# Kernel tuning notes

Hardware: AMD Instinct MI355X
Metric: run time of the kernel (lower is better)

The kernel has to match this reference:

```python
import jax, jax.numpy as jnp
import numpy as np

N = 100000  # nodes per cluster
E = 1000000  # nonzeros per sparse Laplacian
D = 64       # embedding_size
LEAKY_SLOPE = 0.2  # tf.nn.leaky_relu default alpha


def spmm(rows, cols, vals, dense, num_rows):
    """Sparse [num_rows, M] (COO) @ dense [M, D] -> [num_rows, D]."""
    gathered = vals[:, None] * dense[cols]  # [E, D]
    return jax.ops.segment_sum(gathered, rows, num_segments=num_rows)


def setup_inputs() -> dict:
    key = jax.random.key(0)
    ks = jax.random.split(key, 10)
    return {
        "ebs": jax.random.normal(ks[0], (N, D), dtype=jnp.float32),
        "entity_ebs": jax.random.normal(ks[1], (N, D), dtype=jnp.float32),
        "W_side": jax.random.normal(ks[2], (D, D), dtype=jnp.float32),
        "W_dot": jax.random.normal(ks[3], (D, D), dtype=jnp.float32),
        "LI_vals": jax.random.uniform(ks[4], (E,), dtype=jnp.float32),
        "L_vals": jax.random.uniform(ks[5], (E,), dtype=jnp.float32),
        "LI_rows": jax.random.randint(ks[6], (E,), 0, N, dtype=jnp.int32),
        "LI_cols": jax.random.randint(ks[7], (E,), 0, N, dtype=jnp.int32),
        "L_rows": jax.random.randint(ks[8], (E,), 0, N, dtype=jnp.int32),
        "L_cols": jax.random.randint(ks[9], (E,), 0, N, dtype=jnp.int32),
    }


def reference(ebs, entity_ebs, W_side, W_dot, LI_vals, L_vals,
              LI_rows, LI_cols, L_rows, L_cols) -> jnp.ndarray:
    # __build_weight_graph
    LI_side_embed = spmm(LI_rows, LI_cols, LI_vals, ebs, N)   # [N, D]
    L_side_embed = spmm(L_rows, L_cols, L_vals, ebs, N)       # [N, D]
    sum_embed = LI_side_embed @ W_side                          # [N, D]
    dot_embed = (L_side_embed * entity_ebs) @ W_dot             # [N, D]
    return jax.nn.leaky_relu(sum_embed + dot_embed, negative_slope=LEAKY_SLOPE)
```

## Files before the change

kernel.cpp:

```cpp
#include <hip/hip_runtime.h>

#define D        64
#define BINROWS  64
#define SUBCAP   256
#define NSHARD   8
#define NBINS_MAX 1568
#define CHUNK    4096
#define FSTRIDE  68
#define SSEGCAP  2048
#define CURSTRIDE 16

typedef __attribute__((ext_vector_type(8))) short short8;
typedef __attribute__((ext_vector_type(4))) float floatx4;

__device__ __forceinline__ unsigned short f2bf(float f) {
    unsigned u = __float_as_uint(f);
    u += 0x7fffu + ((u >> 16) & 1u);
    return (unsigned short)(u >> 16);
}
__device__ __forceinline__ float bf2f(unsigned short u) {
    return __uint_as_float(((unsigned)u) << 16);
}

__global__ __launch_bounds__(256) void convert_kernel(
    const float* __restrict__ ebs, unsigned short* __restrict__ ebs16, int total4)
{
    int i = blockIdx.x * 256 + threadIdx.x;
    if (i >= total4) return;
    float4 v = ((const float4*)ebs)[i];
    ushort4 o;
    o.x = f2bf(v.x); o.y = f2bf(v.y); o.z = f2bf(v.z); o.w = f2bf(v.w);
    ((ushort4*)ebs16)[i] = o;
}

__global__ __launch_bounds__(256) void wfrag_kernel(
    const float* __restrict__ W_side, const float* __restrict__ W_dot,
    unsigned short* __restrict__ Wfrag)
{
    int t = blockIdx.x * 256 + threadIdx.x;
    int f = t >> 6;
    int l = t & 63;
    int jt = f >> 2, kt = f & 3;
    int q = l >> 4, nl = l & 15;
    int n = jt * 16 + nl;
#pragma unroll
    for (int j = 0; j < 8; ++j) {
        int k = kt * 32 + q * 8 + j;
        float w = (k < 64) ? W_side[k * 64 + n] : W_dot[(k - 64) * 64 + n];
        Wfrag[(size_t)f * 512 + l * 8 + j] = f2bf(w);
    }
}

__global__ __launch_bounds__(256) void expand_bin_kernel(
    const int* __restrict__ LI_rows, const int* __restrict__ LI_cols, const float* __restrict__ LI_vals,
    const int* __restrict__ L_rows,  const int* __restrict__ L_cols,  const float* __restrict__ L_vals,
    int* __restrict__ cursorP, uint2* __restrict__ seg, int E, int nbins)
{
    __shared__ int hist[NBINS_MAX];
    __shared__ int cnt2[NBINS_MAX];
    __shared__ int gbase[NBINS_MAX];

    int t  = threadIdx.x;
    int c0 = blockIdx.x * CHUNK;
    int sh = blockIdx.x & (NSHARD - 1);
    int twoE = 2 * E;

    for (int b = t; b < nbins; b += 256) { hist[b] = 0; cnt2[b] = 0; }
    __syncthreads();

    unsigned rm[CHUNK / 256];
    uint2    cv[CHUNK / 256];

#pragma unroll
    for (int k = 0; k < CHUNK / 256; ++k) {
        int e = c0 + k * 256 + t;
        rm[k] = 0xFFFFFFFFu;
        if (e < twoE) {
            int m = (e >= E) ? 1 : 0;
            int r, cl; float v;
            if (m) { r = L_rows[e - E]; cl = L_cols[e - E]; v = L_vals[e - E]; }
            else   { r = LI_rows[e];    cl = LI_cols[e];    v = LI_vals[e]; }
            rm[k] = (unsigned)r | ((unsigned)m << 17);
            cv[k] = make_uint2((unsigned)cl, __float_as_uint(v));
            atomicAdd(&hist[r >> 6], 1);
        }
    }
    __syncthreads();

    for (int b = t; b < nbins; b += 256) {
        int c = hist[b];
        gbase[b] = c ? atomicAdd(&cursorP[(sh * NBINS_MAX + b) * CURSTRIDE], c) : 0;
    }
    __syncthreads();

#pragma unroll
    for (int k = 0; k < CHUNK / 256; ++k) {
        unsigned g = rm[k];
        if (g == 0xFFFFFFFFu) continue;
        int r   = (int)(g & 0x1FFFFu);
        int m   = (int)((g >> 17) & 1u);
        int bin = r >> 6;
        int rib = r & 63;
        int rank = atomicAdd(&cnt2[bin], 1);
        int pos  = gbase[bin] + rank;
        if (pos < SUBCAP)
            seg[((size_t)(sh * NBINS_MAX) + bin) * SUBCAP + pos] =
                make_uint2(((unsigned)m << 23) | ((unsigned)rib << 17) | cv[k].x, cv[k].y);
    }
}

__global__ __launch_bounds__(256) void fused_kernel(
    const uint2* __restrict__ seg, const int* __restrict__ cursorP,
    const unsigned short* __restrict__ ebs16,
    const float* __restrict__ entity,
    const unsigned short* __restrict__ Wfrag,
    float* __restrict__ out, int n)
{
    __shared__ __align__(16) char shmem[2 * BINROWS * FSTRIDE * 4];
    __shared__ int hist[128];
    __shared__ int offs[128];
    __shared__ int cur[128];
    uint2* sseg = (uint2*)shmem;
    float* facc = (float*)shmem;

    int t = threadIdx.x;
    int b = blockIdx.x;

    if (t < 128) hist[t] = 0;
    __syncthreads();

    int clen[NSHARD];
    uint2 held[NSHARD];
    unsigned hmask = 0;
#pragma unroll
    for (int sh = 0; sh < NSHARD; ++sh) {
        int c = cursorP[(sh * NBINS_MAX + b) * CURSTRIDE];
        clen[sh] = c < SUBCAP ? c : SUBCAP;
        if (t < clen[sh]) {
            held[sh] = seg[((size_t)(sh * NBINS_MAX) + b) * SUBCAP + t];
            hmask |= (1u << sh);
            atomicAdd(&hist[(held[sh].x >> 17) & 127u], 1);
        }
    }
    __syncthreads();

    if (t < 128) offs[t] = hist[t];
    __syncthreads();
    for (int step = 1; step < 128; step <<= 1) {
        int add = 0;
        if (t < 128 && t >= step) add = offs[t - step];
        __syncthreads();
        if (t < 128) offs[t] += add;
        __syncthreads();
    }
    if (t < 128) {
        int excl = offs[t] - hist[t];
        offs[t] = excl;
        cur[t]  = excl;
    }
    __syncthreads();

#pragma unroll
    for (int sh = 0; sh < NSHARD; ++sh) {
        if (hmask & (1u << sh)) {
            unsigned key = (held[sh].x >> 17) & 127u;
            int rank = atomicAdd(&cur[key], 1);
            sseg[rank] = held[sh];
        }
    }
    __syncthreads();

    int g  = t >> 4;
    int l4 = (t & 15) << 2;
    int beg[8], len[8];
    int maxlen = 0;
#pragma unroll
    for (int kk = 0; kk < 8; ++kk) {
        int key = g * 8 + kk;
        beg[kk] = offs[key];
        len[kk] = hist[key];
        maxlen = max(maxlen, len[kk]);
    }
    floatx4 a8[8];
#pragma unroll
    for (int kk = 0; kk < 8; ++kk) a8[kk] = (floatx4){0.f, 0.f, 0.f, 0.f};

    for (int s = 0; s < maxlen; ++s) {
#pragma unroll
        for (int kk = 0; kk < 8; ++kk) {
            if (s < len[kk]) {
                uint2 en = sseg[beg[kk] + s];
                float vv = __uint_as_float(en.y);
                ushort4 x = *(const ushort4*)(ebs16 + (size_t)(en.x & 0x1FFFFu) * D + l4);
                a8[kk][0] += vv * bf2f(x.x);
                a8[kk][1] += vv * bf2f(x.y);
                a8[kk][2] += vv * bf2f(x.z);
                a8[kk][3] += vv * bf2f(x.w);
            }
        }
    }
    __syncthreads();

#pragma unroll
    for (int kk = 0; kk < 8; ++kk) {
        int key = g * 8 + kk;
        float* dst = facc + ((key >> 6) * BINROWS + (key & 63)) * FSTRIDE + l4;
        *(float4*)dst = make_float4(a8[kk][0], a8[kk][1], a8[kk][2], a8[kk][3]);
    }
    __syncthreads();

    int w = t >> 6;
    int l = t & 63;
    int q = l >> 4, mcol = l & 15;
    int rowbase = b * BINROWS + w * 16;
    int growA = rowbase + mcol;
    int binrow = w * 16 + mcol;
    const float* faccLI = facc;
    const float* faccL  = facc + BINROWS * FSTRIDE;

    floatx4 accv[4];
#pragma unroll
    for (int jt = 0; jt < 4; ++jt) accv[jt] = (floatx4){0.f, 0.f, 0.f, 0.f};

#pragma unroll
    for (int kt = 0; kt < 4; ++kt) {
        short8 af;
        if (kt < 2) {
            const float4* ap = (const float4*)(faccLI + binrow * FSTRIDE + kt * 32 + q * 8);
            float4 a0 = ap[0], a1 = ap[1];
            af[0] = (short)f2bf(a0.x); af[1] = (short)f2bf(a0.y);
            af[2] = (short)f2bf(a0.z); af[3] = (short)f2bf(a0.w);
            af[4] = (short)f2bf(a1.x); af[5] = (short)f2bf(a1.y);
            af[6] = (short)f2bf(a1.z); af[7] = (short)f2bf(a1.w);
        } else {
            const float4* lp = (const float4*)(faccL + binrow * FSTRIDE + (kt - 2) * 32 + q * 8);
            float4 l0 = lp[0], l1 = lp[1];
            float4 e0 = make_float4(0.f, 0.f, 0.f, 0.f), e1 = e0;
            if (growA < n) {
                const float4* ep = (const float4*)(entity + (size_t)growA * D + (kt - 2) * 32 + q * 8);
                e0 = ep[0]; e1 = ep[1];
            }
            af[0] = (short)f2bf(l0.x * e0.x); af[1] = (short)f2bf(l0.y * e0.y);
            af[2] = (short)f2bf(l0.z * e0.z); af[3] = (short)f2bf(l0.w * e0.w);
            af[4] = (short)f2bf(l1.x * e1.x); af[5] = (short)f2bf(l1.y * e1.y);
            af[6] = (short)f2bf(l1.z * e1.z); af[7] = (short)f2bf(l1.w * e1.w);
        }
#pragma unroll
        for (int jt = 0; jt < 4; ++jt) {
            const short8 bf = *(const short8*)(Wfrag + (size_t)(jt * 4 + kt) * 512 + (size_t)l * 8);
            accv[jt] = __builtin_amdgcn_mfma_f32_16x16x32_bf16(af, bf, accv[jt], 0, 0, 0);
        }
    }

#pragma unroll
    for (int jt = 0; jt < 4; ++jt) {
#pragma unroll
        for (int r = 0; r < 4; ++r) {
            int grow = rowbase + q * 4 + r;
            if (grow < n) {
                float v = accv[jt][r];
                v = v > 0.f ? v : 0.2f * v;
                out[(size_t)grow * D + jt * 16 + mcol] = v;
            }
        }
    }
}

__global__ void scatter_kernel(
    const float* __restrict__ LI_vals, const int* __restrict__ LI_rows, const int* __restrict__ LI_cols,
    const float* __restrict__ L_vals,  const int* __restrict__ L_rows,  const int* __restrict__ L_cols,
    const float* __restrict__ ebs,
    float* __restrict__ accLI, float* __restrict__ accL, int E)
{
    long long t = (long long)blockIdx.x * blockDim.x + threadIdx.x;
    long long e2 = t >> 4;
    if (e2 >= 2LL * E) return;
    int c = ((int)t & 15) << 2;
    const float* vals; const int* rows; const int* cols; float* acc; int e;
    if (e2 < E) { vals = LI_vals; rows = LI_rows; cols = LI_cols; acc = accLI; e = (int)e2; }
    else        { vals = L_vals;  rows = L_rows;  cols = L_cols;  acc = accL;  e = (int)(e2 - E); }
    float v = vals[e]; int r = rows[e]; int cl = cols[e];
    const float4 x = *(const float4*)(ebs + (size_t)cl * D + c);
    float* o = acc + (size_t)r * D + c;
    unsafeAtomicAdd(o + 0, v * x.x);
    unsafeAtomicAdd(o + 1, v * x.y);
    unsafeAtomicAdd(o + 2, v * x.z);
    unsafeAtomicAdd(o + 3, v * x.w);
}

__global__ __launch_bounds__(256) void epilogue_kernel(
    const float* __restrict__ acc, const float* __restrict__ entity,
    const float* __restrict__ W_side, const float* __restrict__ W_dot,
    float* __restrict__ out, int n)
{
    int lane = threadIdx.x & 63;
    int wave = (blockIdx.x << 2) | (threadIdx.x >> 6);
    int row  = (wave << 6) + lane;
    bool valid = row < n;
    const float* accLI = acc;
    const float* accL  = acc + (size_t)n * D;
    float a[D], b[D];
    if (valid) {
        const float4* ap = (const float4*)(accLI  + (size_t)row * D);
        const float4* lp = (const float4*)(accL   + (size_t)row * D);
        const float4* ep = (const float4*)(entity + (size_t)row * D);
#pragma unroll
        for (int qq = 0; qq < 16; ++qq) {
            float4 av = ap[qq]; float4 lv = lp[qq]; float4 ev = ep[qq];
            a[4*qq+0] = av.x; a[4*qq+1] = av.y; a[4*qq+2] = av.z; a[4*qq+3] = av.w;
            b[4*qq+0] = lv.x * ev.x; b[4*qq+1] = lv.y * ev.y;
            b[4*qq+2] = lv.z * ev.z; b[4*qq+3] = lv.w * ev.w;
        }
    } else {
#pragma unroll
        for (int qq = 0; qq < D; ++qq) { a[qq] = 0.f; b[qq] = 0.f; }
    }
    float4* op = (float4*)(out + (size_t)row * D);
#pragma unroll 1
    for (int jc = 0; jc < 16; ++jc) {
        float a0 = 0.f, a1 = 0.f, a2 = 0.f, a3 = 0.f;
#pragma unroll
        for (int k = 0; k < D; ++k) {
            float4 w1 = *(const float4*)(W_side + (k << 6) + (jc << 2));
            float4 w2 = *(const float4*)(W_dot  + (k << 6) + (jc << 2));
            a0 += a[k] * w1.x + b[k] * w2.x;
            a1 += a[k] * w1.y + b[k] * w2.y;
            a2 += a[k] * w1.z + b[k] * w2.z;
            a3 += a[k] * w1.w + b[k] * w2.w;
        }
        float4 r;
        r.x = a0 > 0.f ? a0 : 0.2f * a0;
        r.y = a1 > 0.f ? a1 : 0.2f * a1;
        r.z = a2 > 0.f ? a2 : 0.2f * a2;
        r.w = a3 > 0.f ? a3 : 0.2f * a3;
        if (valid) op[jc] = r;
    }
}

extern "C" void kernel_launch(void* const* d_in, const int* in_sizes, int n_in,
                              void* d_out, int out_size, void* d_ws, size_t ws_size,
                              hipStream_t stream) {
    const float* ebs     = (const float*)d_in[0];
    const float* entity  = (const float*)d_in[1];
    const float* W_side  = (const float*)d_in[2];
    const float* W_dot   = (const float*)d_in[3];
    const float* LI_vals = (const float*)d_in[4];
    const float* L_vals  = (const float*)d_in[5];
    const int*   LI_rows = (const int*)d_in[6];
    const int*   LI_cols = (const int*)d_in[7];
    const int*   L_rows  = (const int*)d_in[8];
    const int*   L_cols  = (const int*)d_in[9];
    float* out = (float*)d_out;

    int E = in_sizes[4];
    int n = in_sizes[0] / D;
    int nbins = (n + BINROWS - 1) / BINROWS;

    size_t curBytes = (size_t)NSHARD * NBINS_MAX * CURSTRIDE * sizeof(int);
    size_t segBytes = (size_t)NSHARD * NBINS_MAX * SUBCAP * sizeof(uint2);
    size_t ebsBytes = (size_t)n * D * sizeof(unsigned short);
    size_t wfBytes  = (size_t)16 * 512 * sizeof(unsigned short);
    size_t need = curBytes + segBytes + ebsBytes + wfBytes;

    if (ws_size >= need && nbins <= NBINS_MAX && n <= 131072) {
        int*            cursorP = (int*)d_ws;
        uint2*          seg     = (uint2*)((char*)d_ws + curBytes);
        unsigned short* ebs16   = (unsigned short*)((char*)d_ws + curBytes + segBytes);
        unsigned short* Wfrag   = (unsigned short*)((char*)d_ws + curBytes + segBytes + ebsBytes);

        hipMemsetAsync(cursorP, 0, curBytes, stream);

        int total4 = n * D / 4;
        convert_kernel<<<(total4 + 255) / 256, 256, 0, stream>>>(ebs, ebs16, total4);
        wfrag_kernel<<<4, 256, 0, stream>>>(W_side, W_dot, Wfrag);

        int xblocks = (2 * E + CHUNK - 1) / CHUNK;
        expand_bin_kernel<<<xblocks, 256, 0, stream>>>(
            LI_rows, LI_cols, LI_vals, L_rows, L_cols, L_vals,
            cursorP, seg, E, nbins);

        fused_kernel<<<nbins, 256, 0, stream>>>(
            seg, cursorP, ebs16, entity, Wfrag, out, n);
    } else {
        size_t accBytes = (size_t)2 * n * D * sizeof(float);
        float* acc   = (float*)d_ws;
        float* accLI = acc;
        float* accL  = accLI + (size_t)n * D;
        hipMemsetAsync(d_ws, 0, accBytes, stream);
        long long totalThreads = 2LL * E * 16;
        int sblocks = (int)((totalThreads + 255) / 256);
        scatter_kernel<<<sblocks, 256, 0, stream>>>(
            LI_vals, LI_rows, LI_cols, L_vals, L_rows, L_cols, ebs, accLI, accL, E);
        int nTiles = (n + 63) / 64;
        epilogue_kernel<<<(nTiles + 3) / 4, 256, 0, stream>>>(
            acc, entity, W_side, W_dot, out, n);
    }
}
```

Measured before the change: 272.6 us.

## Locally sort edges by bin before scatter; branchless predicated gathers in fused SpMM

The expand kernel now counting-sorts each chunk's edges by bin in shared memory, using a block prefix scan, and then writes them out in sorted order. Consecutive threads therefore write contiguous segments of each bin's buffer instead of scattering randomly. The fused kernel's inner gather loop drops its per-entry branch: inactive lanes read a clamped index with zero weight, so all eight independent gathers can be issued together. The cost is extra shared memory and syncs in the expand kernel, and wasted gathers of row 0 when bins are unbalanced.

```diff
diff --git a/kernel.cpp b/kernel.cpp
--- a/kernel.cpp
+++ b/kernel.cpp
@@ -6,6 +6,7 @@
 #define NSHARD   8
 #define NBINS_MAX 1568
 #define CHUNK    4096
+#define PER_TH   (CHUNK / 256)
 #define FSTRIDE  68
 #define SSEGCAP  2048
 #define CURSTRIDE 16
@@ -56,23 +57,28 @@
     const int* __restrict__ L_rows,  const int* __restrict__ L_cols,  const float* __restrict__ L_vals,
     int* __restrict__ cursorP, uint2* __restrict__ seg, int E, int nbins)
 {
+    __shared__ uint2 sorted[CHUNK];
+    __shared__ unsigned short sbin[CHUNK];
     __shared__ int hist[NBINS_MAX];
-    __shared__ int cnt2[NBINS_MAX];
+    __shared__ int offs[NBINS_MAX];
+    __shared__ int cur[NBINS_MAX];
     __shared__ int gbase[NBINS_MAX];
+    __shared__ int tsum[256];
 
     int t  = threadIdx.x;
     int c0 = blockIdx.x * CHUNK;
     int sh = blockIdx.x & (NSHARD - 1);
     int twoE = 2 * E;
-
-    for (int b = t; b < nbins; b += 256) { hist[b] = 0; cnt2[b] = 0; }
-    __syncthreads();
-
-    unsigned rm[CHUNK / 256];
-    uint2    cv[CHUNK / 256];
-
-#pragma unroll
-    for (int k = 0; k < CHUNK / 256; ++k) {
+    int chunkcnt = twoE - c0; if (chunkcnt > CHUNK) chunkcnt = CHUNK;
+
+    for (int b = t; b < NBINS_MAX; b += 256) hist[b] = 0;
+    __syncthreads();
+
+    unsigned rm[PER_TH];
+    uint2    cv[PER_TH];
+
+#pragma unroll
+    for (int k = 0; k < PER_TH; ++k) {
         int e = c0 + k * 256 + t;
         rm[k] = 0xFFFFFFFFu;
         if (e < twoE) {
@@ -87,25 +93,54 @@
     }
     __syncthreads();
 
+    int loc[7]; int tot = 0;
+    if (t < 224) {
+#pragma unroll
+        for (int i = 0; i < 7; ++i) { loc[i] = tot; tot += hist[t * 7 + i]; }
+    }
+    tsum[t] = (t < 224) ? tot : 0;
+    __syncthreads();
+    for (int step = 1; step < 256; step <<= 1) {
+        int add = (t >= step) ? tsum[t - step] : 0;
+        __syncthreads();
+        tsum[t] += add;
+        __syncthreads();
+    }
+    int tbase = tsum[t] - ((t < 224) ? tot : 0);
+    if (t < 224) {
+#pragma unroll
+        for (int i = 0; i < 7; ++i) {
+            int key = t * 7 + i;
+            int o = tbase + loc[i];
+            offs[key] = o;
+            cur[key]  = o;
+        }
+    }
+    __syncthreads();
+
     for (int b = t; b < nbins; b += 256) {
         int c = hist[b];
         gbase[b] = c ? atomicAdd(&cursorP[(sh * NBINS_MAX + b) * CURSTRIDE], c) : 0;
     }
-    __syncthreads();
-
-#pragma unroll
-    for (int k = 0; k < CHUNK / 256; ++k) {
+
+#pragma unroll
+    for (int k = 0; k < PER_TH; ++k) {
         unsigned g = rm[k];
         if (g == 0xFFFFFFFFu) continue;
         int r   = (int)(g & 0x1FFFFu);
         int m   = (int)((g >> 17) & 1u);
         int bin = r >> 6;
-        int rib = r & 63;
-        int rank = atomicAdd(&cnt2[bin], 1);
-        int pos  = gbase[bin] + rank;
+        int rank = atomicAdd(&cur[bin], 1);
+        sorted[rank] = make_uint2(((unsigned)m << 23) | ((unsigned)(r & 63) << 17) | cv[k].x, cv[k].y);
+        sbin[rank]   = (unsigned short)bin;
+    }
+    __syncthreads();
+
+    for (int i = t; i < chunkcnt; i += 256) {
+        int bin = sbin[i];
+        int pos = gbase[bin] + (i - offs[bin]);
         if (pos < SUBCAP)
-            seg[((size_t)(sh * NBINS_MAX) + bin) * SUBCAP + pos] =
-                make_uint2(((unsigned)m << 23) | ((unsigned)rib << 17) | cv[k].x, cv[k].y);
+            seg[((size_t)(sh * NBINS_MAX) + bin) * SUBCAP + pos] = sorted[i];
     }
 }
 
@@ -172,13 +207,14 @@
 
     int g  = t >> 4;
     int l4 = (t & 15) << 2;
-    int beg[8], len[8];
+    int beg[8], len[8], lenm1[8];
     int maxlen = 0;
 #pragma unroll
     for (int kk = 0; kk < 8; ++kk) {
         int key = g * 8 + kk;
-        beg[kk] = offs[key];
-        len[kk] = hist[key];
+        beg[kk]   = offs[key];
+        len[kk]   = hist[key];
+        lenm1[kk] = len[kk] > 0 ? len[kk] - 1 : 0;
         maxlen = max(maxlen, len[kk]);
     }
     floatx4 a8[8];
@@ -188,15 +224,16 @@
     for (int s = 0; s < maxlen; ++s) {
 #pragma unroll
         for (int kk = 0; kk < 8; ++kk) {
-            if (s < len[kk]) {
-                uint2 en = sseg[beg[kk] + s];
-                float vv = __uint_as_float(en.y);
-                ushort4 x = *(const ushort4*)(ebs16 + (size_t)(en.x & 0x1FFFFu) * D + l4);
-                a8[kk][0] += vv * bf2f(x.x);
-                a8[kk][1] += vv * bf2f(x.y);
-                a8[kk][2] += vv * bf2f(x.z);
-                a8[kk][3] += vv * bf2f(x.w);
-            }
+            bool sel = s < len[kk];
+            int idx  = beg[kk] + min(s, lenm1[kk]);
+            uint2 en = sseg[idx];
+            unsigned enx = sel ? en.x : 0u;
+            float vv = sel ? __uint_as_float(en.y) : 0.f;
+            ushort4 x = *(const ushort4*)(ebs16 + (size_t)(enx & 0x1FFFFu) * D + l4);
+            a8[kk][0] += vv * bf2f(x.x);
+            a8[kk][1] += vv * bf2f(x.y);
+            a8[kk][2] += vv * bf2f(x.z);
+            a8[kk][3] += vv * bf2f(x.w);
         }
     }
     __syncthreads();
```

Result: faster. 226.7 us (-16.8%).
